# Kernel optimization log

Hardware: AMD Instinct MI355X
Metric: run time of the kernel (lower is better)

Reference implementation:

```python
import math
import jax, jax.numpy as jnp
import numpy as np

NUM_CLASSES = 722
BLUR_RANGE = 3

def _gaussian_val(dist, sigma=1):
    # matches torch module: exp(-2**dist / (2 * 2**sigma))
    return math.exp(-math.pow(2, dist) / (2 * math.pow(2, sigma)))

def setup_inputs() -> dict:
    key = jax.random.key(0)
    k1, k2 = jax.random.split(key)
    pred = jax.random.normal(k1, (16, 4096, NUM_CLASSES), dtype=jnp.float32)
    target = jax.random.randint(k2, (16, 4096), 0, NUM_CLASSES, dtype=jnp.int64)
    return {"pred": pred, "target": target}

def _smoothed_label(target):
    # Replicates the exact sequence of scatter_(value) overwrites, including
    cls = jnp.arange(NUM_CLASSES)  # [C]
    sm = jnp.zeros(target.shape + (NUM_CLASSES,), dtype=jnp.float32)
    for dist in range(BLUR_RANGE, -1, -1):
        val = jnp.float32(_gaussian_val(dist))
        for idx in (jnp.clip(target - dist, 0, NUM_CLASSES - 1),
                    jnp.clip(target + dist, 0, NUM_CLASSES - 1)):
            sm = jnp.where(cls == idx[..., None], val, sm)
    # final scatter of exactly 1.0 at the target index
    sm = jnp.where(cls == target[..., None], jnp.float32(1.0), sm)
    return sm

def reference(pred, target):
    logp = jax.nn.log_softmax(pred, axis=-1)          # [B,S,C]
    sm = _smoothed_label(target)                      # [B,S,C], constant
    return jnp.mean(jnp.sum(-logp * sm, axis=-1))
```

## Files before the change

### kernel.cpp

```cpp
#include <hip/hip_runtime.h>
#include <math.h>

#define NUM_CLASSES 722
#define NROWS 65536
#define F2_PER_ROW 361
#define ROWS_PER_BLOCK 4
#define GRID1 (NROWS / ROWS_PER_BLOCK)

#define W1 0.60653065971263342f
#define W2 0.36787944117144233f
#define W3 0.13533528323661270f

__global__ __launch_bounds__(256) void ce_rows_kernel(
    const float* __restrict__ pred,
    const int*   __restrict__ target,
    float*       __restrict__ block_sums)
{
    const int wave = threadIdx.x >> 6;
    const int lane = threadIdx.x & 63;
    const int row  = blockIdx.x * ROWS_PER_BLOCK + wave;

    const float2* rowp = reinterpret_cast<const float2*>(pred) + (size_t)row * F2_PER_ROW;

    float2 v[6];
    float m = -INFINITY;
#pragma unroll
    for (int k = 0; k < 6; ++k) {
        int idx = lane + k * 64;
        v[k] = make_float2(0.f, 0.f);
        if (idx < F2_PER_ROW) {
            v[k] = rowp[idx];
            m = fmaxf(m, fmaxf(v[k].x, v[k].y));
        }
    }
#pragma unroll
    for (int off = 32; off >= 1; off >>= 1)
        m = fmaxf(m, __shfl_xor(m, off, 64));

    const int t  = target[row];
    const int p1 = min(t + 1, NUM_CLASSES - 1), q1 = max(t - 1, 0);
    const int p2 = min(t + 2, NUM_CLASSES - 1), q2 = max(t - 2, 0);
    const int p3 = min(t + 3, NUM_CLASSES - 1), q3 = max(t - 3, 0);

    float s = 0.f, dot = 0.f, wsum = 0.f;
#pragma unroll
    for (int k = 0; k < 6; ++k) {
        int idx = lane + k * 64;
        if (idx < F2_PER_ROW) {
            int c0 = idx * 2, c1 = c0 + 1;
            s += __expf(v[k].x - m) + __expf(v[k].y - m);
            float w0 = (c0 == t)  ? 1.0f :
                       (c0 == p1) ? W1 : (c0 == q1) ? W1 :
                       (c0 == p2) ? W2 : (c0 == q2) ? W2 :
                       (c0 == p3) ? W3 : (c0 == q3) ? W3 : 0.0f;
            float w1 = (c1 == t)  ? 1.0f :
                       (c1 == p1) ? W1 : (c1 == q1) ? W1 :
                       (c1 == p2) ? W2 : (c1 == q2) ? W2 :
                       (c1 == p3) ? W3 : (c1 == q3) ? W3 : 0.0f;
            dot  += w0 * v[k].x + w1 * v[k].y;
            wsum += w0 + w1;
        }
    }
#pragma unroll
    for (int off = 32; off >= 1; off >>= 1) {
        s    += __shfl_xor(s,    off, 64);
        dot  += __shfl_xor(dot,  off, 64);
        wsum += __shfl_xor(wsum, off, 64);
    }

    __shared__ float lds[ROWS_PER_BLOCK];
    if (lane == 0) {
        float lse = m + __logf(s);
        lds[wave] = lse * wsum - dot;
    }
    __syncthreads();
    if (threadIdx.x == 0)
        block_sums[blockIdx.x] = lds[0] + lds[1] + lds[2] + lds[3];
}

__global__ __launch_bounds__(1024) void reduce_final_kernel(
    const float* __restrict__ block_sums,
    float*       __restrict__ out,
    int n)
{
    float s = 0.f;
    for (int i = threadIdx.x; i < n; i += 1024)
        s += block_sums[i];
#pragma unroll
    for (int off = 32; off >= 1; off >>= 1)
        s += __shfl_xor(s, off, 64);

    __shared__ float lds[16];
    const int wave = threadIdx.x >> 6, lane = threadIdx.x & 63;
    if (lane == 0) lds[wave] = s;
    __syncthreads();
    if (threadIdx.x == 0) {
        float tot = 0.f;
#pragma unroll
        for (int i = 0; i < 16; ++i) tot += lds[i];
        out[0] = tot * (1.0f / (float)NROWS);
    }
}

extern "C" void kernel_launch(void* const* d_in, const int* in_sizes, int n_in,
                              void* d_out, int out_size, void* d_ws, size_t ws_size,
                              hipStream_t stream)
{
    const float* pred   = (const float*)d_in[0];
    const int*   target = (const int*)d_in[1];
    float* out        = (float*)d_out;
    float* block_sums = (float*)d_ws;

    ce_rows_kernel<<<GRID1, 256, 0, stream>>>(pred, target, block_sums);
    reduce_final_kernel<<<1, 1024, 0, stream>>>(block_sums, out, GRID1);
}
```

Before: 263.0 us.

## Use float4 row loads and gather the seven smoothed-label logits directly

Rows are now loaded as 16-byte float4 vectors, using a per-row parity offset to keep the loads aligned, plus an extra float2 covering the leftover pair. Instead of computing weights for all 722 classes with compare chains and reducing dot and wsum across the wave, each lane gathers the seven logits at the clamped target neighbours and accumulates the weighted sum with deduplication. This cuts per-element ALU work and two shuffle reductions and makes the loads wider. In exchange it adds redundant scalar gathers in every lane and relies on the parity-based alignment logic being correct.

```diff
diff --git a/kernel.cpp b/kernel.cpp
--- a/kernel.cpp
+++ b/kernel.cpp
@@ -3,7 +3,6 @@
 
 #define NUM_CLASSES 722
 #define NROWS 65536
-#define F2_PER_ROW 361
 #define ROWS_PER_BLOCK 4
 #define GRID1 (NROWS / ROWS_PER_BLOCK)
 
@@ -20,53 +19,54 @@
     const int lane = threadIdx.x & 63;
     const int row  = blockIdx.x * ROWS_PER_BLOCK + wave;
 
-    const float2* rowp = reinterpret_cast<const float2*>(pred) + (size_t)row * F2_PER_ROW;
+    const float* base = pred + (size_t)row * NUM_CLASSES;
 
-    float2 v[6];
-    float m = -INFINITY;
-#pragma unroll
-    for (int k = 0; k < 6; ++k) {
-        int idx = lane + k * 64;
-        v[k] = make_float2(0.f, 0.f);
-        if (idx < F2_PER_ROW) {
-            v[k] = rowp[idx];
-            m = fmaxf(m, fmaxf(v[k].x, v[k].y));
-        }
-    }
+    const int t  = target[row];
+    const int c0 = t;
+    const int c1 = min(t + 1, NUM_CLASSES - 1), c2 = max(t - 1, 0);
+    const int c3 = min(t + 2, NUM_CLASSES - 1), c4 = max(t - 2, 0);
+    const int c5 = min(t + 3, NUM_CLASSES - 1), c6 = max(t - 3, 0);
+    const float g0 = base[c0], g1 = base[c1], g2 = base[c2], g3 = base[c3],
+                g4 = base[c4], g5 = base[c5], g6 = base[c6];
+
+    const int p = row & 1;
+    const float4* v4 = reinterpret_cast<const float4*>(base + 2 * p);
+    const float NEG_INF = -INFINITY;
+
+    float4 v[3];
+    v[0] = v4[lane];
+    v[1] = v4[lane + 64];
+    v[2] = make_float4(NEG_INF, NEG_INF, NEG_INF, NEG_INF);
+    if (lane < 52) v[2] = v4[lane + 128];
+    float2 ex = make_float2(NEG_INF, NEG_INF);
+    if (lane == 63) ex = reinterpret_cast<const float2*>(base)[p ? 0 : 360];
+
+    float m = fmaxf(fmaxf(fmaxf(v[0].x, v[0].y), fmaxf(v[0].z, v[0].w)),
+                    fmaxf(fmaxf(v[1].x, v[1].y), fmaxf(v[1].z, v[1].w)));
+    m = fmaxf(m, fmaxf(fmaxf(v[2].x, v[2].y), fmaxf(v[2].z, v[2].w)));
+    m = fmaxf(m, fmaxf(ex.x, ex.y));
 #pragma unroll
     for (int off = 32; off >= 1; off >>= 1)
         m = fmaxf(m, __shfl_xor(m, off, 64));
 
-    const int t  = target[row];
-    const int p1 = min(t + 1, NUM_CLASSES - 1), q1 = max(t - 1, 0);
-    const int p2 = min(t + 2, NUM_CLASSES - 1), q2 = max(t - 2, 0);
-    const int p3 = min(t + 3, NUM_CLASSES - 1), q3 = max(t - 3, 0);
+    float s = __expf(v[0].x - m) + __expf(v[0].y - m)
+            + __expf(v[0].z - m) + __expf(v[0].w - m)
+            + __expf(v[1].x - m) + __expf(v[1].y - m)
+            + __expf(v[1].z - m) + __expf(v[1].w - m)
+            + __expf(v[2].x - m) + __expf(v[2].y - m)
+            + __expf(v[2].z - m) + __expf(v[2].w - m)
+            + __expf(ex.x - m)   + __expf(ex.y - m);
+#pragma unroll
+    for (int off = 32; off >= 1; off >>= 1)
+        s += __shfl_xor(s, off, 64);
 
-    float s = 0.f, dot = 0.f, wsum = 0.f;
-#pragma unroll
-    for (int k = 0; k < 6; ++k) {
-        int idx = lane + k * 64;
-        if (idx < F2_PER_ROW) {
-            int c0 = idx * 2, c1 = c0 + 1;
-            s += __expf(v[k].x - m) + __expf(v[k].y - m);
-            float w0 = (c0 == t)  ? 1.0f :
-                       (c0 == p1) ? W1 : (c0 == q1) ? W1 :
-                       (c0 == p2) ? W2 : (c0 == q2) ? W2 :
-                       (c0 == p3) ? W3 : (c0 == q3) ? W3 : 0.0f;
-            float w1 = (c1 == t)  ? 1.0f :
-                       (c1 == p1) ? W1 : (c1 == q1) ? W1 :
-                       (c1 == p2) ? W2 : (c1 == q2) ? W2 :
-                       (c1 == p3) ? W3 : (c1 == q3) ? W3 : 0.0f;
-            dot  += w0 * v[k].x + w1 * v[k].y;
-            wsum += w0 + w1;
-        }
-    }
-#pragma unroll
-    for (int off = 32; off >= 1; off >>= 1) {
-        s    += __shfl_xor(s,    off, 64);
-        dot  += __shfl_xor(dot,  off, 64);
-        wsum += __shfl_xor(wsum, off, 64);
-    }
+    float dot = g0, wsum = 1.0f;
+    if (c1 != c0) { dot += W1 * g1; wsum += W1; }
+    if (c2 != c0 && c2 != c1) { dot += W1 * g2; wsum += W1; }
+    if (c3 != c0 && c3 != c1 && c3 != c2) { dot += W2 * g3; wsum += W2; }
+    if (c4 != c0 && c4 != c1 && c4 != c2 && c4 != c3) { dot += W2 * g4; wsum += W2; }
+    if (c5 != c0 && c5 != c1 && c5 != c2 && c5 != c3 && c5 != c4) { dot += W3 * g5; wsum += W3; }
+    if (c6 != c0 && c6 != c1 && c6 != c2 && c6 != c3 && c6 != c4 && c6 != c5) { dot += W3 * g6; wsum += W3; }
 
     __shared__ float lds[ROWS_PER_BLOCK];
     if (lane == 0) {
```

After: 257.2 us. 2.2% less time.
